# Performance work log

Measured on AMD Instinct MI355X. Metric: run time of the kernel, lower is better.

Reference implementation:

```python
import jax, jax.numpy as jnp
import numpy as np

H = 1024          # hidden_dim; also the attention 'sequence' length (embed_dim=1)
L = 12            # n_layers per stack (att1 and att2 each have L blocks)
FF = 4 * H        # MLP expansion
B, CT_DIM, CL_DIM = 8, 2048, 128
EPS = 1e-5


def _ln(x, g, b):
    m = jnp.mean(x, axis=-1, keepdims=True)
    v = jnp.mean((x - m) ** 2, axis=-1, keepdims=True)
    return (x - m) / jnp.sqrt(v + EPS) * g + b


def setup_inputs() -> dict:
    key = jax.random.key(0)
    ks = jax.random.split(key, 8)

    def w(k, shape, s=0.02):
        return (jax.random.normal(k, shape) * s).astype(jnp.float32)

    inp = {
        "ct": jax.random.normal(ks[0], (B, CT_DIM), jnp.float32),
        "clinical": jax.random.normal(ks[1], (B, CL_DIM), jnp.float32),
        "W_ct": w(ks[2], (CT_DIM, H)), "b_ct": jnp.zeros((H,), jnp.float32),
        "W_cl": w(ks[3], (CL_DIM, H)), "b_cl": jnp.zeros((H,), jnp.float32),
        "norm_g": jnp.ones((2 * H,), jnp.float32),
        "norm_b": jnp.zeros((2 * H,), jnp.float32),
    }
    for i, pre in enumerate(("att1", "att2")):
        kk = jax.random.split(ks[4 + i], 4)
        inp[pre + "_inw"] = w(kk[0], (L, 3), 0.5)      # q,k,v scalar in-proj weights (embed_dim=1)
        inp[pre + "_inb"] = jnp.zeros((L, 3), jnp.float32)
        inp[pre + "_ow"] = w(kk[1], (L,), 0.5)          # scalar out-proj weight
        inp[pre + "_ob"] = jnp.zeros((L,), jnp.float32)
        inp[pre + "_g1"] = jnp.ones((L, H), jnp.float32)
        inp[pre + "_be1"] = jnp.zeros((L, H), jnp.float32)
        inp[pre + "_g2"] = jnp.ones((L, H), jnp.float32)
        inp[pre + "_be2"] = jnp.zeros((L, H), jnp.float32)
        inp[pre + "_W1"] = w(kk[2], (L, H, FF))
        inp[pre + "_b1"] = jnp.zeros((L, FF), jnp.float32)
        inp[pre + "_W2"] = w(kk[3], (L, FF, H))
        inp[pre + "_b2"] = jnp.zeros((L, H), jnp.float32)
    return inp


def _stack(query, kv, params):
    # query is fixed across the stack; kv is the carried state (matches
    # Scale_Dot_Attention returning (query, kv, kv) through nn.Sequential).
    def step(kv, p):
        inw, inb, ow, ob, g1, be1, g2, be2, W1, b1, W2, b2 = p
        v = _ln(kv, g1, be1)                              # norm1(value)  [B,H]
        # embed_dim=1 MHA: scalar in-projections, scale = 1/sqrt(1) = 1
        qp = query * inw[0] + inb[0]                      # [B,H]
        kp = kv * inw[1] + inb[1]                         # [B,H]
        vp = v * inw[2] + inb[2]                          # [B,H]
        attn = jax.nn.softmax(qp[:, :, None] * kp[:, None, :], axis=-1)  # [B,H,H]
        av = jnp.einsum('bqk,bk->bq', attn, vp) * ow + ob                # out-proj
        out = _ln(av + v, g2, be2)                        # norm2(attn + normed value)
        out = out + jax.nn.gelu(out @ W1 + b1, approximate=False) @ W2 + b2
        return out, None
    kv, _ = jax.lax.scan(step, kv, params)
    return kv


def _forward(ct, clinical, W_ct, b_ct, W_cl, b_cl,
             att1_inw, att1_inb, att1_ow, att1_ob, att1_g1, att1_be1,
             att1_g2, att1_be2, att1_W1, att1_b1, att1_W2, att1_b2,
             att2_inw, att2_inb, att2_ow, att2_ob, att2_g1, att2_be1,
             att2_g2, att2_be2, att2_W1, att2_b1, att2_W2, att2_b2,
             norm_g, norm_b):
    cte = ct @ W_ct + b_ct            # [B,H]
    cle = clinical @ W_cl + b_cl      # [B,H]
    p1 = (att1_inw, att1_inb, att1_ow, att1_ob, att1_g1, att1_be1,
          att1_g2, att1_be2, att1_W1, att1_b1, att1_W2, att1_b2)
    p2 = (att2_inw, att2_inb, att2_ow, att2_ob, att2_g1, att2_be1,
          att2_g2, att2_be2, att2_W1, att2_b1, att2_W2, att2_b2)
    ct_attn = _stack(cle, cte, p1)    # att1: query=clinical, kv=ct
    cl_attn = _stack(cte, cle, p2)    # att2: query=ct, kv=clinical
    return _ln(jnp.concatenate([ct_attn, cl_attn], axis=1), norm_g, norm_b)


def reference(ct, clinical, W_ct, b_ct, W_cl, b_cl,
              att1_inw, att1_inb, att1_ow, att1_ob, att1_g1, att1_be1,
              att1_g2, att1_be2, att1_W1, att1_b1, att1_W2, att1_b2,
              att2_inw, att2_inb, att2_ow, att2_ob, att2_g1, att2_be1,
              att2_g2, att2_be2, att2_W1, att2_b1, att2_W2, att2_b2,
              norm_g, norm_b):
    return _forward(ct, clinical, W_ct, b_ct, W_cl, b_cl,
                    att1_inw, att1_inb, att1_ow, att1_ob, att1_g1, att1_be1,
                    att1_g2, att1_be2, att1_W1, att1_b1, att1_W2, att1_b2,
                    att2_inw, att2_inb, att2_ow, att2_ob, att2_g1, att2_be1,
                    att2_g2, att2_be2, att2_W1, att2_b1, att2_W2, att2_b2,
                    norm_g, norm_b)
```

## Files before the change

### kernel.cpp

```cpp
#include <hip/hip_runtime.h>
#include <cstddef>

namespace {

constexpr int kH = 1024;
constexpr int kFF = 4096;
constexpr int kB = 8;
constexpr int kL = 12;
constexpr float kEps = 1e-5f;

struct StackParams {
  const float *inw, *inb, *ow, *ob, *g1, *be1, *g2, *be2, *W1, *b1, *W2, *b2;
};

__device__ __forceinline__ void blkReduceSum2(float& a, float& c, float* red) {
#pragma unroll
  for (int m = 1; m < 64; m <<= 1) { a += __shfl_xor(a, m); c += __shfl_xor(c, m); }
  int w = threadIdx.x >> 6;
  __syncthreads();
  if ((threadIdx.x & 63) == 0) { red[w] = a; red[4 + w] = c; }
  __syncthreads();
  a = red[0] + red[1] + red[2] + red[3];
  c = red[4] + red[5] + red[6] + red[7];
}

__device__ __forceinline__ void blkReduceMaxMin(float& a, float& c, float* red) {
#pragma unroll
  for (int m = 1; m < 64; m <<= 1) {
    a = fmaxf(a, __shfl_xor(a, m));
    c = fminf(c, __shfl_xor(c, m));
  }
  int w = threadIdx.x >> 6;
  __syncthreads();
  if ((threadIdx.x & 63) == 0) { red[w] = a; red[4 + w] = c; }
  __syncthreads();
  a = fmaxf(fmaxf(red[0], red[1]), fmaxf(red[2], red[3]));
  c = fminf(fminf(red[4], red[5]), fminf(red[6], red[7]));
}

template <int KC>
__global__ __launch_bounds__(256) void gemvPart(const float* __restrict__ X,
                                                const float* __restrict__ W,
                                                float* __restrict__ part,
                                                int K, int N) {
  const int FT = N >> 10;
  int ft = blockIdx.x % FT;
  int kc = blockIdx.x / FT;
  int k0 = kc * KC;
  __shared__ float Xs[kB][KC];
  int t = threadIdx.x;
  for (int i = t; i < kB * KC; i += 256) {
    int b = i / KC, kk = i % KC;
    Xs[b][kk] = X[(size_t)b * K + k0 + kk];
  }
  __syncthreads();
  int c0 = (ft << 10) + (t << 2);
  float acc[kB][4];
#pragma unroll
  for (int b = 0; b < kB; ++b)
#pragma unroll
    for (int j = 0; j < 4; ++j) acc[b][j] = 0.f;
  const float* Wp = W + (size_t)k0 * N + c0;
#pragma unroll
  for (int kk = 0; kk < KC; ++kk) {
    float4 w = *reinterpret_cast<const float4*>(Wp + (size_t)kk * N);
#pragma unroll
    for (int b = 0; b < kB; ++b) {
      float x = Xs[b][kk];
      acc[b][0] = fmaf(x, w.x, acc[b][0]);
      acc[b][1] = fmaf(x, w.y, acc[b][1]);
      acc[b][2] = fmaf(x, w.z, acc[b][2]);
      acc[b][3] = fmaf(x, w.w, acc[b][3]);
    }
  }
  float* pp = part + (size_t)kc * kB * N + c0;
#pragma unroll
  for (int b = 0; b < kB; ++b) {
    *reinterpret_cast<float4*>(pp + (size_t)b * N) =
        make_float4(acc[b][0], acc[b][1], acc[b][2], acc[b][3]);
  }
}

__global__ __launch_bounds__(256) void embedReduce(const float* __restrict__ pct,
                                                   const float* __restrict__ pcl,
                                                   const float* __restrict__ b_ct,
                                                   const float* __restrict__ b_cl,
                                                   float* __restrict__ emb,
                                                   float* __restrict__ kv) {
  int id = blockIdx.x * 256 + threadIdx.x;
  int s = id >> 13;
  int bn = id & 8191;
  int n = id & 1023;
  float sum;
  if (s == 0) {
    sum = b_ct[n];
#pragma unroll 4
    for (int p = 0; p < 128; ++p) sum += pct[(size_t)p * 8192 + bn];
  } else {
    sum = b_cl[n];
#pragma unroll 4
    for (int p = 0; p < 32; ++p) sum += pcl[(size_t)p * 8192 + bn];
  }
  emb[id] = sum;
  kv[id] = sum;
}

__global__ __launch_bounds__(256) void attnKernel(const float* __restrict__ kv,
                                                  const float* __restrict__ emb,
                                                  float* __restrict__ y2,
                                                  StackParams P0, StackParams P1,
                                                  int l) {
  int bid = blockIdx.x;
  int s = bid >> 8;
  int b = (bid >> 5) & 7;
  int qt = bid & 31;
  StackParams P = s ? P1 : P0;
  const float* kvr = kv + ((size_t)((s << 3) + b)) * kH;
  const float* qr = emb + ((size_t)(((1 - s) << 3) + b)) * kH;
  float wi0 = P.inw[l * 3 + 0], wi1 = P.inw[l * 3 + 1], wi2 = P.inw[l * 3 + 2];
  float bi0 = P.inb[l * 3 + 0], bi1 = P.inb[l * 3 + 1], bi2 = P.inb[l * 3 + 2];
  float ow = P.ow[l], ob = P.ob[l];
  const float* g1 = P.g1 + (size_t)l * kH;
  const float* be1 = P.be1 + (size_t)l * kH;

  __shared__ float kvs[kH];
  __shared__ float2 kvp[kH];
  __shared__ float red[8];

  int t = threadIdx.x;
  float lsum = 0.f, lsq = 0.f;
#pragma unroll
  for (int i = 0; i < 4; ++i) {
    float x = kvr[t + 256 * i];
    kvs[t + 256 * i] = x;
    lsum += x;
    lsq += x * x;
  }
  blkReduceSum2(lsum, lsq, red);
  float mean = lsum * (1.f / kH);
  float rstd = rsqrtf(lsq * (1.f / kH) - mean * mean + kEps);

  float lmax = -1e30f, lmin = 1e30f;
#pragma unroll
  for (int i = 0; i < 4; ++i) {
    int k = t + 256 * i;
    float x = kvs[k];
    float kp = fmaf(x, wi1, bi1);
    float v = (x - mean) * rstd * g1[k] + be1[k];
    float vp = fmaf(v, wi2, bi2);
    kvp[k] = make_float2(kp, vp);
    lmax = fmaxf(lmax, kp);
    lmin = fminf(lmin, kp);
  }
  blkReduceMaxMin(lmax, lmin, red);
  __syncthreads();

  int q = (qt << 5) + (t >> 3);
  int ks = t & 7;
  float sq = fmaf(qr[q], wi0, bi0);
  float mb = fmaxf(sq * lmax, sq * lmin);
  float den0 = 0.f, num0 = 0.f, den1 = 0.f, num1 = 0.f;
#pragma unroll 4
  for (int j = 0; j < 128; j += 2) {
    float2 a = kvp[ks + (j << 3)];
    float2 c = kvp[ks + ((j + 1) << 3)];
    float e0 = __expf(fmaf(sq, a.x, -mb));
    float e1 = __expf(fmaf(sq, c.x, -mb));
    den0 += e0; num0 = fmaf(e0, a.y, num0);
    den1 += e1; num1 = fmaf(e1, c.y, num1);
  }
  float den = den0 + den1, num = num0 + num1;
#pragma unroll
  for (int m = 1; m < 8; m <<= 1) {
    den += __shfl_xor(den, m);
    num += __shfl_xor(num, m);
  }
  if (ks == 0) {
    float av = num / den;
    float vq = (kvs[q] - mean) * rstd * g1[q] + be1[q];
    y2[((size_t)((s << 3) + b)) * kH + q] = fmaf(av, ow, ob) + vq;
  }
}

__global__ __launch_bounds__(256) void gemm1Kernel(const float* __restrict__ y2,
                                                   float* __restrict__ xn,
                                                   float* __restrict__ part1,
                                                   StackParams P0, StackParams P1,
                                                   int l) {
  int bid = blockIdx.x;
  int s = bid >> 8;
  int ft = (bid >> 6) & 3;
  int kc = bid & 63;
  StackParams P = s ? P1 : P0;
  const float* y2s = y2 + ((size_t)s << 13);
  __shared__ float sm[kB], sr[kB];
  __shared__ float Xs[kB][16];
  int t = threadIdx.x;
  {
    int b = t >> 5, lane = t & 31;
    const float* row = y2s + (size_t)b * kH;
    float sum = 0.f, sq = 0.f;
    for (int i = lane; i < kH; i += 32) {
      float x = row[i];
      sum += x;
      sq += x * x;
    }
#pragma unroll
    for (int m = 1; m < 32; m <<= 1) { sum += __shfl_xor(sum, m); sq += __shfl_xor(sq, m); }
    if (lane == 0) {
      float mean = sum * (1.f / kH);
      sm[b] = mean;
      sr[b] = rsqrtf(sq * (1.f / kH) - mean * mean + kEps);
    }
  }
  __syncthreads();
  int k0 = kc << 4;
  if (t < 128) {
    int b = t >> 4, kk = t & 15, k = k0 + kk;
    float x = y2s[(size_t)b * kH + k];
    float v = (x - sm[b]) * sr[b] * P.g2[(size_t)l * kH + k] + P.be2[(size_t)l * kH + k];
    Xs[b][kk] = v;
    if (ft == 0) xn[((size_t)s << 13) + (size_t)b * kH + k] = v;
  }
  __syncthreads();
  int c0 = (ft << 10) + (t << 2);
  const float* W = P.W1 + (size_t)l * kH * kFF + (size_t)k0 * kFF + c0;
  float acc[kB][4];
#pragma unroll
  for (int b = 0; b < kB; ++b)
#pragma unroll
    for (int j = 0; j < 4; ++j) acc[b][j] = 0.f;
#pragma unroll
  for (int kk = 0; kk < 16; ++kk) {
    float4 w = *reinterpret_cast<const float4*>(W + (size_t)kk * kFF);
#pragma unroll
    for (int b = 0; b < kB; ++b) {
      float x = Xs[b][kk];
      acc[b][0] = fmaf(x, w.x, acc[b][0]);
      acc[b][1] = fmaf(x, w.y, acc[b][1]);
      acc[b][2] = fmaf(x, w.z, acc[b][2]);
      acc[b][3] = fmaf(x, w.w, acc[b][3]);
    }
  }
  float* pp = part1 + ((size_t)(s * 64 + kc) * kB) * kFF + c0;
#pragma unroll
  for (int b = 0; b < kB; ++b) {
    *reinterpret_cast<float4*>(pp + (size_t)b * kFF) =
        make_float4(acc[b][0], acc[b][1], acc[b][2], acc[b][3]);
  }
}

__global__ __launch_bounds__(256) void gemm2Kernel(const float* __restrict__ part1,
                                                   float* __restrict__ part2,
                                                   StackParams P0, StackParams P1,
                                                   int l) {
  int bid = blockIdx.x;
  int s = bid >> 8;
  int kc = bid & 255;
  StackParams P = s ? P1 : P0;
  int k0 = kc << 4;
  __shared__ float Xs[kB][16];
  int t = threadIdx.x;
  if (t < 128) {
    int b = t >> 4, kk = t & 15;
    const float* pp = part1 + (size_t)s * 64 * kB * kFF + (size_t)b * kFF + k0 + kk;
    float sum = P.b1[(size_t)l * kFF + k0 + kk];
#pragma unroll 8
    for (int p = 0; p < 64; ++p) sum += pp[(size_t)p * kB * kFF];
    Xs[b][kk] = 0.5f * sum * (1.f + erff(sum * 0.70710678118654752f));
  }
  __syncthreads();
  int c0 = t << 2;
  const float* W = P.W2 + (size_t)l * kFF * kH + (size_t)k0 * kH + c0;
  float acc[kB][4];
#pragma unroll
  for (int b = 0; b < kB; ++b)
#pragma unroll
    for (int j = 0; j < 4; ++j) acc[b][j] = 0.f;
#pragma unroll
  for (int kk = 0; kk < 16; ++kk) {
    float4 w = *reinterpret_cast<const float4*>(W + (size_t)kk * kH);
#pragma unroll
    for (int b = 0; b < kB; ++b) {
      float x = Xs[b][kk];
      acc[b][0] = fmaf(x, w.x, acc[b][0]);
      acc[b][1] = fmaf(x, w.y, acc[b][1]);
      acc[b][2] = fmaf(x, w.z, acc[b][2]);
      acc[b][3] = fmaf(x, w.w, acc[b][3]);
    }
  }
  float* pp = part2 + ((size_t)(s * 256 + kc) * kB) * kH + c0;
#pragma unroll
  for (int b = 0; b < kB; ++b) {
    *reinterpret_cast<float4*>(pp + (size_t)b * kH) =
        make_float4(acc[b][0], acc[b][1], acc[b][2], acc[b][3]);
  }
}

__global__ __launch_bounds__(256) void reduce2Kernel(const float* __restrict__ part2,
                                                     const float* __restrict__ xn,
                                                     float* __restrict__ kv,
                                                     StackParams P0, StackParams P1,
                                                     int l) {
  int gid = blockIdx.x * 256 + threadIdx.x;
  int o = gid >> 2;
  int ks = gid & 3;
  int s = o >> 13;
  int bn = o & 8191;
  int n = o & 1023;
  const float* pp = part2 + (size_t)s * 256 * 8192 + (size_t)ks * 8192 + bn;
  float sum = 0.f;
#pragma unroll 8
  for (int j = 0; j < 64; ++j) sum += pp[(size_t)j * 4 * 8192];
  sum += __shfl_xor(sum, 1);
  sum += __shfl_xor(sum, 2);
  if (ks == 0) {
    StackParams P = s ? P1 : P0;
    kv[o] = sum + P.b2[(size_t)l * kH + n] + xn[o];
  }
}

__global__ __launch_bounds__(256) void finalLn(const float* __restrict__ kv,
                                               const float* __restrict__ g,
                                               const float* __restrict__ bb,
                                               float* __restrict__ out) {
  int b = blockIdx.x;
  int t = threadIdx.x;
  __shared__ float red[8];
  float vals[8];
  float sum = 0.f, sq = 0.f;
#pragma unroll
  for (int i = 0; i < 8; ++i) {
    int idx = t + 256 * i;
    int s = idx >> 10, n = idx & 1023;
    float x = kv[(size_t)s * 8192 + (size_t)b * kH + n];
    vals[i] = x;
    sum += x;
    sq += x * x;
  }
  blkReduceSum2(sum, sq, red);
  float mean = sum * (1.f / 2048.f);
  float rstd = rsqrtf(sq * (1.f / 2048.f) - mean * mean + kEps);
#pragma unroll
  for (int i = 0; i < 8; ++i) {
    int idx = t + 256 * i;
    out[(size_t)b * 2048 + idx] = (vals[i] - mean) * rstd * g[idx] + bb[idx];
  }
}

}

extern "C" void kernel_launch(void* const* d_in, const int* in_sizes, int n_in,
                              void* d_out, int out_size, void* d_ws, size_t ws_size,
                              hipStream_t stream) {
  const float* ct = (const float*)d_in[0];
  const float* clinical = (const float*)d_in[1];
  const float* W_ct = (const float*)d_in[2];
  const float* b_ct = (const float*)d_in[3];
  const float* W_cl = (const float*)d_in[4];
  const float* b_cl = (const float*)d_in[5];
  const float* norm_g = (const float*)d_in[6];
  const float* norm_b = (const float*)d_in[7];

  StackParams P0{(const float*)d_in[8],  (const float*)d_in[9],  (const float*)d_in[10],
                 (const float*)d_in[11], (const float*)d_in[12], (const float*)d_in[13],
                 (const float*)d_in[14], (const float*)d_in[15], (const float*)d_in[16],
                 (const float*)d_in[17], (const float*)d_in[18], (const float*)d_in[19]};
  StackParams P1{(const float*)d_in[20], (const float*)d_in[21], (const float*)d_in[22],
                 (const float*)d_in[23], (const float*)d_in[24], (const float*)d_in[25],
                 (const float*)d_in[26], (const float*)d_in[27], (const float*)d_in[28],
                 (const float*)d_in[29], (const float*)d_in[30], (const float*)d_in[31]};

  float* ws = (float*)d_ws;
  float* emb = ws;
  float* kv = emb + 2 * kB * kH;
  float* y2 = kv + 2 * kB * kH;
  float* xn = y2 + 2 * kB * kH;
  float* part1 = xn + 2 * kB * kH;
  float* part2 = part1 + (size_t)2 * 64 * kB * kFF;
  float* pct = part1;
  float* pcl = part1 + (size_t)128 * kB * kH;

  gemvPart<16><<<128, 256, 0, stream>>>(ct, W_ct, pct, 2048, 1024);
  gemvPart<4><<<32, 256, 0, stream>>>(clinical, W_cl, pcl, 128, 1024);
  embedReduce<<<64, 256, 0, stream>>>(pct, pcl, b_ct, b_cl, emb, kv);

  for (int l = 0; l < kL; ++l) {
    attnKernel<<<512, 256, 0, stream>>>(kv, emb, y2, P0, P1, l);
    gemm1Kernel<<<512, 256, 0, stream>>>(y2, xn, part1, P0, P1, l);
    gemm2Kernel<<<512, 256, 0, stream>>>(part1, part2, P0, P1, l);
    reduce2Kernel<<<256, 256, 0, stream>>>(part2, xn, kv, P0, P1, l);
  }

  finalLn<<<8, 256, 0, stream>>>(kv, norm_g, norm_b, (float*)d_out);
}
```

Measured before the change: 627.8 us.

## Reduce split-K partials in-block and fold final reduction into attention

The GEMM tiling is restructured so each block covers 256 rows of K instead of 16. Partial sums are reduced inside the block through shuffles and shared memory, which cuts the partial buffers from 64/256 slices to 4/16. The reduce2 kernel is removed: attention (and the final LayerNorm) now sum the 16 part2 slices plus bias and residual on the fly, saving one launch per layer and a large amount of partial-sum traffic. In exchange it adds LDS reduction work and syncs, and every attention block redundantly sums its row's partials.

Result: faster. 578.4 us (-7.9%).

```diff
diff --git a/kernel.cpp b/kernel.cpp
--- a/kernel.cpp
+++ b/kernel.cpp
@@ -86,7 +86,7 @@
                                                    const float* __restrict__ b_ct,
                                                    const float* __restrict__ b_cl,
                                                    float* __restrict__ emb,
-                                                   float* __restrict__ kv) {
+                                                   float* __restrict__ kv0) {
   int id = blockIdx.x * 256 + threadIdx.x;
   int s = id >> 13;
   int bn = id & 8191;
@@ -102,10 +102,12 @@
     for (int p = 0; p < 32; ++p) sum += pcl[(size_t)p * 8192 + bn];
   }
   emb[id] = sum;
-  kv[id] = sum;
-}
-
-__global__ __launch_bounds__(256) void attnKernel(const float* __restrict__ kv,
+  kv0[id] = sum;
+}
+
+__global__ __launch_bounds__(256) void attnKernel(const float* __restrict__ kv0,
+                                                  const float* __restrict__ part2,
+                                                  const float* __restrict__ xn,
                                                   const float* __restrict__ emb,
                                                   float* __restrict__ y2,
                                                   StackParams P0, StackParams P1,
@@ -115,7 +117,6 @@
   int b = (bid >> 5) & 7;
   int qt = bid & 31;
   StackParams P = s ? P1 : P0;
-  const float* kvr = kv + ((size_t)((s << 3) + b)) * kH;
   const float* qr = emb + ((size_t)(((1 - s) << 3) + b)) * kH;
   float wi0 = P.inw[l * 3 + 0], wi1 = P.inw[l * 3 + 1], wi2 = P.inw[l * 3 + 2];
   float bi0 = P.inb[l * 3 + 0], bi1 = P.inb[l * 3 + 1], bi2 = P.inb[l * 3 + 2];
@@ -129,12 +130,30 @@
 
   int t = threadIdx.x;
   float lsum = 0.f, lsq = 0.f;
-#pragma unroll
-  for (int i = 0; i < 4; ++i) {
-    float x = kvr[t + 256 * i];
-    kvs[t + 256 * i] = x;
-    lsum += x;
-    lsq += x * x;
+  if (l == 0) {
+    const float* kvr = kv0 + ((size_t)((s << 3) + b)) * kH;
+#pragma unroll
+    for (int i = 0; i < 4; ++i) {
+      int n = t + 256 * i;
+      float x = kvr[n];
+      kvs[n] = x;
+      lsum += x;
+      lsq += x * x;
+    }
+  } else {
+    const float* b2p = P.b2 + (size_t)(l - 1) * kH;
+    const float* xr = xn + ((size_t)((s << 3) + b)) * kH;
+    const float* pp = part2 + ((size_t)(s * 16) * kB + b) * kH;
+#pragma unroll
+    for (int i = 0; i < 4; ++i) {
+      int n = t + 256 * i;
+      float x = b2p[n] + xr[n];
+#pragma unroll 4
+      for (int p = 0; p < 16; ++p) x += pp[(size_t)p * kB * kH + n];
+      kvs[n] = x;
+      lsum += x;
+      lsq += x * x;
+    }
   }
   blkReduceSum2(lsum, lsq, red);
   float mean = lsum * (1.f / kH);
@@ -182,6 +201,37 @@
   }
 }
 
+__device__ __forceinline__ float4 tileReduce(float acc[kB][4], float* red, int t) {
+#pragma unroll
+  for (int b = 0; b < kB; ++b)
+#pragma unroll
+    for (int j = 0; j < 4; ++j) {
+      float v = acc[b][j];
+      v += __shfl_xor(v, 16);
+      v += __shfl_xor(v, 32);
+      acc[b][j] = v;
+    }
+  int wave = t >> 6, lane = t & 63;
+  if (lane < 16) {
+#pragma unroll
+    for (int b = 0; b < kB; ++b) {
+      float* p = red + (size_t)(wave * 16 + lane) * 40 + b * 4;
+      p[0] = acc[b][0]; p[1] = acc[b][1]; p[2] = acc[b][2]; p[3] = acc[b][3];
+    }
+  }
+  __syncthreads();
+  float4 sum = make_float4(0.f, 0.f, 0.f, 0.f);
+  if (t < 128) {
+    int cq = t >> 3, b = t & 7;
+#pragma unroll
+    for (int w = 0; w < 4; ++w) {
+      const float* p = red + (size_t)(w * 16 + cq) * 40 + b * 4;
+      sum.x += p[0]; sum.y += p[1]; sum.z += p[2]; sum.w += p[3];
+    }
+  }
+  return sum;
+}
+
 __global__ __launch_bounds__(256) void gemm1Kernel(const float* __restrict__ y2,
                                                    float* __restrict__ xn,
                                                    float* __restrict__ part1,
@@ -189,12 +239,13 @@
                                                    int l) {
   int bid = blockIdx.x;
   int s = bid >> 8;
-  int ft = (bid >> 6) & 3;
-  int kc = bid & 63;
+  int kc = (bid >> 6) & 3;
+  int ft = bid & 63;
   StackParams P = s ? P1 : P0;
   const float* y2s = y2 + ((size_t)s << 13);
   __shared__ float sm[kB], sr[kB];
-  __shared__ float Xs[kB][16];
+  __shared__ float Xs[kB][256];
+  __shared__ float red[64 * 40];
   int t = threadIdx.x;
   {
     int b = t >> 5, lane = t & 31;
@@ -214,39 +265,45 @@
     }
   }
   __syncthreads();
-  int k0 = kc << 4;
-  if (t < 128) {
-    int b = t >> 4, kk = t & 15, k = k0 + kk;
-    float x = y2s[(size_t)b * kH + k];
-    float v = (x - sm[b]) * sr[b] * P.g2[(size_t)l * kH + k] + P.be2[(size_t)l * kH + k];
+  int k0 = kc << 8;
+  const float* g2p = P.g2 + (size_t)l * kH + k0;
+  const float* be2p = P.be2 + (size_t)l * kH + k0;
+#pragma unroll
+  for (int i = 0; i < 8; ++i) {
+    int idx = t + 256 * i;
+    int b = idx >> 8, kk = idx & 255;
+    float x = y2s[(size_t)b * kH + k0 + kk];
+    float v = (x - sm[b]) * sr[b] * g2p[kk] + be2p[kk];
     Xs[b][kk] = v;
-    if (ft == 0) xn[((size_t)s << 13) + (size_t)b * kH + k] = v;
-  }
-  __syncthreads();
-  int c0 = (ft << 10) + (t << 2);
-  const float* W = P.W1 + (size_t)l * kH * kFF + (size_t)k0 * kFF + c0;
+    if (ft == 0) xn[((size_t)((s << 3) + b)) * kH + k0 + kk] = v;
+  }
+  __syncthreads();
+  int cq = t & 15, rg = t >> 4;
+  int c0 = (ft << 6) + (cq << 2);
+  const float* W = P.W1 + (size_t)l * kH * kFF + (size_t)(k0 + rg) * kFF + c0;
   float acc[kB][4];
 #pragma unroll
   for (int b = 0; b < kB; ++b)
 #pragma unroll
     for (int j = 0; j < 4; ++j) acc[b][j] = 0.f;
 #pragma unroll
-  for (int kk = 0; kk < 16; ++kk) {
-    float4 w = *reinterpret_cast<const float4*>(W + (size_t)kk * kFF);
+  for (int i = 0; i < 16; ++i) {
+    float4 w = *reinterpret_cast<const float4*>(W + (size_t)i * 16 * kFF);
+    int r = rg + 16 * i;
 #pragma unroll
     for (int b = 0; b < kB; ++b) {
-      float x = Xs[b][kk];
+      float x = Xs[b][r];
       acc[b][0] = fmaf(x, w.x, acc[b][0]);
       acc[b][1] = fmaf(x, w.y, acc[b][1]);
       acc[b][2] = fmaf(x, w.z, acc[b][2]);
       acc[b][3] = fmaf(x, w.w, acc[b][3]);
     }
   }
-  float* pp = part1 + ((size_t)(s * 64 + kc) * kB) * kFF + c0;
-#pragma unroll
-  for (int b = 0; b < kB; ++b) {
-    *reinterpret_cast<float4*>(pp + (size_t)b * kFF) =
-        make_float4(acc[b][0], acc[b][1], acc[b][2], acc[b][3]);
+  float4 sum = tileReduce(acc, red, t);
+  if (t < 128) {
+    int cqq = t >> 3, b = t & 7;
+    float* pp = part1 + ((size_t)((s * 4 + kc) * kB + b)) * kFF + (ft << 6) + (cqq << 2);
+    *reinterpret_cast<float4*>(pp) = sum;
   }
 }
 
@@ -256,94 +313,90 @@
                                                    int l) {
   int bid = blockIdx.x;
   int s = bid >> 8;
-  int kc = bid & 255;
+  int kc = (bid >> 4) & 15;
+  int ft = bid & 15;
   StackParams P = s ? P1 : P0;
-  int k0 = kc << 4;
-  __shared__ float Xs[kB][16];
+  int k0 = kc << 8;
+  __shared__ float Xs[kB][256];
+  __shared__ float red[64 * 40];
   int t = threadIdx.x;
-  if (t < 128) {
-    int b = t >> 4, kk = t & 15;
-    const float* pp = part1 + (size_t)s * 64 * kB * kFF + (size_t)b * kFF + k0 + kk;
-    float sum = P.b1[(size_t)l * kFF + k0 + kk];
-#pragma unroll 8
-    for (int p = 0; p < 64; ++p) sum += pp[(size_t)p * kB * kFF];
+  const float* b1p = P.b1 + (size_t)l * kFF + k0;
+#pragma unroll
+  for (int i = 0; i < 8; ++i) {
+    int idx = t + 256 * i;
+    int b = idx >> 8, kk = idx & 255;
+    const float* pp = part1 + ((size_t)(s * 4) * kB + b) * kFF + k0 + kk;
+    float sum = b1p[kk];
+#pragma unroll
+    for (int p = 0; p < 4; ++p) sum += pp[(size_t)p * kB * kFF];
     Xs[b][kk] = 0.5f * sum * (1.f + erff(sum * 0.70710678118654752f));
   }
   __syncthreads();
-  int c0 = t << 2;
-  const float* W = P.W2 + (size_t)l * kFF * kH + (size_t)k0 * kH + c0;
+  int cq = t & 15, rg = t >> 4;
+  int c0 = (ft << 6) + (cq << 2);
+  const float* W = P.W2 + (size_t)l * kFF * kH + (size_t)(k0 + rg) * kH + c0;
   float acc[kB][4];
 #pragma unroll
   for (int b = 0; b < kB; ++b)
 #pragma unroll
     for (int j = 0; j < 4; ++j) acc[b][j] = 0.f;
 #pragma unroll
-  for (int kk = 0; kk < 16; ++kk) {
-    float4 w = *reinterpret_cast<const float4*>(W + (size_t)kk * kH);
+  for (int i = 0; i < 16; ++i) {
+    float4 w = *reinterpret_cast<const float4*>(W + (size_t)i * 16 * kH);
+    int r = rg + 16 * i;
 #pragma unroll
     for (int b = 0; b < kB; ++b) {
-      float x = Xs[b][kk];
+      float x = Xs[b][r];
       acc[b][0] = fmaf(x, w.x, acc[b][0]);
       acc[b][1] = fmaf(x, w.y, acc[b][1]);
       acc[b][2] = fmaf(x, w.z, acc[b][2]);
       acc[b][3] = fmaf(x, w.w, acc[b][3]);
     }
   }
-  float* pp = part2 + ((size_t)(s * 256 + kc) * kB) * kH + c0;
-#pragma unroll
-  for (int b = 0; b < kB; ++b) {
-    *reinterpret_cast<float4*>(pp + (size_t)b * kH) =
-        make_float4(acc[b][0], acc[b][1], acc[b][2], acc[b][3]);
-  }
-}
-
-__global__ __launch_bounds__(256) void reduce2Kernel(const float* __restrict__ part2,
-                                                     const float* __restrict__ xn,
-                                                     float* __restrict__ kv,
-                                                     StackParams P0, StackParams P1,
-                                                     int l) {
-  int gid = blockIdx.x * 256 + threadIdx.x;
-  int o = gid >> 2;
-  int ks = gid & 3;
-  int s = o >> 13;
-  int bn = o & 8191;
-  int n = o & 1023;
-  const float* pp = part2 + (size_t)s * 256 * 8192 + (size_t)ks * 8192 + bn;
-  float sum = 0.f;
-#pragma unroll 8
-  for (int j = 0; j < 64; ++j) sum += pp[(size_t)j * 4 * 8192];
-  sum += __shfl_xor(sum, 1);
-  sum += __shfl_xor(sum, 2);
-  if (ks == 0) {
-    StackParams P = s ? P1 : P0;
-    kv[o] = sum + P.b2[(size_t)l * kH + n] + xn[o];
-  }
-}
-
-__global__ __launch_bounds__(256) void finalLn(const float* __restrict__ kv,
-                                               const float* __restrict__ g,
-                                               const float* __restrict__ bb,
-                                               float* __restrict__ out) {
+  float4 sum = tileReduce(acc, red, t);
+  if (t < 128) {
+    int cqq = t >> 3, b = t & 7;
+    float* pp = part2 + ((size_t)((s * 16 + kc) * kB + b)) * kH + (ft << 6) + (cqq << 2);
+    *reinterpret_cast<float4*>(pp) = sum;
+  }
+}
+
+__global__ __launch_bounds__(1024) void finalLn(const float* __restrict__ part2,
+                                                const float* __restrict__ xn,
+                                                const float* __restrict__ g,
+                                                const float* __restrict__ bb,
+                                                StackParams P0, StackParams P1,
+                                                float* __restrict__ out) {
   int b = blockIdx.x;
   int t = threadIdx.x;
-  __shared__ float red[8];
-  float vals[8];
+  __shared__ float red[32];
+  float vals[2];
   float sum = 0.f, sq = 0.f;
 #pragma unroll
-  for (int i = 0; i < 8; ++i) {
-    int idx = t + 256 * i;
-    int s = idx >> 10, n = idx & 1023;
-    float x = kv[(size_t)s * 8192 + (size_t)b * kH + n];
+  for (int i = 0; i < 2; ++i) {
+    int s = i, n = t;
+    StackParams P = s ? P1 : P0;
+    float x = P.b2[(size_t)(kL - 1) * kH + n] + xn[((size_t)((s << 3) + b)) * kH + n];
+    const float* pp = part2 + ((size_t)(s * 16) * kB + b) * kH + n;
+#pragma unroll 4
+    for (int p = 0; p < 16; ++p) x += pp[(size_t)p * kB * kH];
     vals[i] = x;
     sum += x;
     sq += x * x;
   }
-  blkReduceSum2(sum, sq, red);
+#pragma unroll
+  for (int m = 1; m < 64; m <<= 1) { sum += __shfl_xor(sum, m); sq += __shfl_xor(sq, m); }
+  int w = t >> 6;
+  if ((t & 63) == 0) { red[w] = sum; red[16 + w] = sq; }
+  __syncthreads();
+  sum = 0.f; sq = 0.f;
+#pragma unroll
+  for (int j = 0; j < 16; ++j) { sum += red[j]; sq += red[16 + j]; }
   float mean = sum * (1.f / 2048.f);
   float rstd = rsqrtf(sq * (1.f / 2048.f) - mean * mean + kEps);
 #pragma unroll
-  for (int i = 0; i < 8; ++i) {
-    int idx = t + 256 * i;
+  for (int i = 0; i < 2; ++i) {
+    int idx = t + 1024 * i;
     out[(size_t)b * 2048 + idx] = (vals[i] - mean) * rstd * g[idx] + bb[idx];
   }
 }
@@ -373,24 +426,23 @@
 
   float* ws = (float*)d_ws;
   float* emb = ws;
-  float* kv = emb + 2 * kB * kH;
-  float* y2 = kv + 2 * kB * kH;
+  float* kv0 = emb + 2 * kB * kH;
+  float* y2 = kv0 + 2 * kB * kH;
   float* xn = y2 + 2 * kB * kH;
   float* part1 = xn + 2 * kB * kH;
-  float* part2 = part1 + (size_t)2 * 64 * kB * kFF;
-  float* pct = part1;
-  float* pcl = part1 + (size_t)128 * kB * kH;
+  float* part2 = part1 + (size_t)2 * 4 * kB * kFF;
+  float* pct = part2 + (size_t)2 * 16 * kB * kH;
+  float* pcl = pct + (size_t)128 * kB * kH;
 
   gemvPart<16><<<128, 256, 0, stream>>>(ct, W_ct, pct, 2048, 1024);
   gemvPart<4><<<32, 256, 0, stream>>>(clinical, W_cl, pcl, 128, 1024);
-  embedReduce<<<64, 256, 0, stream>>>(pct, pcl, b_ct, b_cl, emb, kv);
+  embedReduce<<<64, 256, 0, stream>>>(pct, pcl, b_ct, b_cl, emb, kv0);
 
   for (int l = 0; l < kL; ++l) {
-    attnKernel<<<512, 256, 0, stream>>>(kv, emb, y2, P0, P1, l);
+    attnKernel<<<512, 256, 0, stream>>>(kv0, part2, xn, emb, y2, P0, P1, l);
     gemm1Kernel<<<512, 256, 0, stream>>>(y2, xn, part1, P0, P1, l);
     gemm2Kernel<<<512, 256, 0, stream>>>(part1, part2, P0, P1, l);
-    reduce2Kernel<<<256, 256, 0, stream>>>(part2, xn, kv, P0, P1, l);
-  }
-
-  finalLn<<<8, 256, 0, stream>>>(kv, norm_g, norm_b, (float*)d_out);
-}
+  }
+
+  finalLn<<<8, 1024, 0, stream>>>(part2, xn, norm_g, norm_b, P0, P1, (float*)d_out);
+}
```
